# Performance work log

Hardware: AMD Instinct MI355X
Metric: run time of the kernel (lower is better)

The kernel has to match this reference:

```python
import jax, jax.numpy as jnp
import numpy as np

N_NODES = 100000
N_EDGES = 1600000
IN_C = 128
HID_C = 128   # 2 * out_channels
OUT_C = 64


def gcn_conv(x, row, col, w, W, b, num_nodes):
    """PyG GCNConv: linear transform, add self-loops (weight 1),
    symmetric degree normalization, scatter-sum aggregation, bias."""
    h = x @ W  # [N, C_out]
    loop = jnp.arange(num_nodes, dtype=row.dtype)
    r = jnp.concatenate([row, loop])
    c = jnp.concatenate([col, loop])
    ew = jnp.concatenate([w, jnp.ones((num_nodes,), dtype=w.dtype)])
    deg = jax.ops.segment_sum(ew, c, num_segments=num_nodes)
    dinv = jnp.where(deg > 0, jax.lax.rsqrt(deg), 0.0)
    norm = dinv[r] * ew * dinv[c]            # [E+N]
    msg = h[r] * norm[:, None]               # [E+N, C_out] gather
    out = jax.ops.segment_sum(msg, c, num_segments=num_nodes)
    return out + b


def setup_inputs() -> dict:
    key = jax.random.key(0)
    k1, k2, k3, k4, k5, k6, k7, k8 = jax.random.split(key, 8)
    x = jax.random.normal(k1, (N_NODES, IN_C), dtype=jnp.float32)
    edge_index = jax.random.randint(k2, (2, N_EDGES), 0, N_NODES, dtype=jnp.int64)
    edge_weight = jax.random.uniform(k3, (N_EDGES,), dtype=jnp.float32)
    s1 = float(np.sqrt(6.0 / (IN_C + HID_C)))
    s2 = float(np.sqrt(6.0 / (HID_C + OUT_C)))
    W1 = jax.random.uniform(k4, (IN_C, HID_C), minval=-s1, maxval=s1, dtype=jnp.float32)
    b1 = jnp.zeros((HID_C,), dtype=jnp.float32)
    W2 = jax.random.uniform(k5, (HID_C, OUT_C), minval=-s2, maxval=s2, dtype=jnp.float32)
    b2 = jnp.zeros((OUT_C,), dtype=jnp.float32)
    return {"x": x, "edge_index": edge_index, "edge_weight": edge_weight,
            "W1": W1, "b1": b1, "W2": W2, "b2": b2}


def reference(x, edge_index, edge_weight, W1, b1, W2, b2):
    row, col = edge_index[0], edge_index[1]
    n = x.shape[0]
    h = jax.nn.relu(gcn_conv(x, row, col, edge_weight, W1, b1, n))
    h = jax.nn.relu(gcn_conv(h, row, col, edge_weight, W2, b2, n))
    return h
```

## Files before the change

kernel.cpp:

```cpp
#include <hip/hip_runtime.h>

#define TPB 256

typedef unsigned int uint32;
typedef unsigned short ushort_t;
typedef __attribute__((ext_vector_type(8))) short bf16x8;
typedef __attribute__((ext_vector_type(4))) float f32x4;

constexpr int NB = 256;
constexpr int B1 = 256;

__device__ __forceinline__ uint32 pack_bf16x2(float a, float b) {
  uint32 ua = __float_as_uint(a), ub = __float_as_uint(b);
  ua += 0x7FFFu + ((ua >> 16) & 1u);
  ub += 0x7FFFu + ((ub >> 16) & 1u);
  return (ua >> 16) | (ub & 0xFFFF0000u);
}
__device__ __forceinline__ ushort_t bf16_of(float a) {
  uint32 u = __float_as_uint(a);
  u += 0x7FFFu + ((u >> 16) & 1u);
  return (ushort_t)(u >> 16);
}
__device__ __forceinline__ float bf16_lo(uint32 u) { return __uint_as_float(u << 16); }
__device__ __forceinline__ float bf16_hi(uint32 u) { return __uint_as_float(u & 0xFFFF0000u); }
__device__ __forceinline__ int edge_src(uint32 e) { return (int)(e >> 15); }
__device__ __forceinline__ float edge_w(uint32 e) { return __uint_as_float((e & 0x7FFFu) << 16); }
__device__ __forceinline__ float ubf0(uint32 u) { return (float)(u & 0xFFu); }
__device__ __forceinline__ float ubf1(uint32 u) { return (float)((u >> 8) & 0xFFu); }
__device__ __forceinline__ float ubf2(uint32 u) { return (float)((u >> 16) & 0xFFu); }
__device__ __forceinline__ float ubf3(uint32 u) { return (float)((u >> 24) & 0xFFu); }

__global__ __launch_bounds__(256) void rx_hist(const int* __restrict__ col,
                                               int* __restrict__ blockhist, int e, int chunk,
                                               const float* __restrict__ W1, ushort_t* __restrict__ Wt1,
                                               const float* __restrict__ W2, ushort_t* __restrict__ Wt2,
                                               const float* __restrict__ b1, float* __restrict__ b1p) {
  __shared__ int h[NB];
  int tid = threadIdx.x, blk = blockIdx.x;
  h[tid] = 0;
  __syncthreads();
  int s = blk * chunk, t = min(e, s + chunk);
  for (int i = s + tid; i < t; i += 256) atomicAdd(&h[col[i] & 255], 1);
  int gtid = blk * 256 + tid;
  if (gtid < 128 * 128) {
    int k = gtid >> 7, m = gtid & 127;
    Wt1[m * 128 + k] = bf16_of(W1[gtid]);
  } else if (gtid < 128 * 128 + 128 * 64) {
    int j = gtid - 128 * 128;
    int k = j >> 6, m = j & 63;
    int kp = ((k & 15) << 3) | (k >> 4);
    Wt2[m * 128 + kp] = bf16_of(W2[j]);
  } else if (gtid < 128 * 128 + 128 * 64 + 128) {
    int p = gtid - (128 * 128 + 128 * 64);
    b1p[p] = b1[16 * (p & 7) + (p >> 3)];
  }
  __syncthreads();
  blockhist[tid * B1 + blk] = h[tid];
}

__global__ __launch_bounds__(256) void k_scan1(int* __restrict__ a, int* __restrict__ bsum, int n) {
  __shared__ int s[256];
  int tid = threadIdx.x;
  int base = blockIdx.x * 1024 + tid * 4;
  int v0 = 0, v1 = 0, v2 = 0, v3 = 0;
  if (base + 0 < n) v0 = a[base + 0];
  if (base + 1 < n) v1 = a[base + 1];
  if (base + 2 < n) v2 = a[base + 2];
  if (base + 3 < n) v3 = a[base + 3];
  int tsum = v0 + v1 + v2 + v3;
  s[tid] = tsum;
  __syncthreads();
  for (int off = 1; off < 256; off <<= 1) {
    int t = (tid >= off) ? s[tid - off] : 0;
    __syncthreads();
    s[tid] += t;
    __syncthreads();
  }
  if (tid == 255) bsum[blockIdx.x] = s[255];
  int e0 = s[tid] - tsum;
  int e1 = e0 + v0, e2 = e1 + v1, e3 = e2 + v2;
  if (base + 0 < n) a[base + 0] = e0;
  if (base + 1 < n) a[base + 1] = e1;
  if (base + 2 < n) a[base + 2] = e2;
  if (base + 3 < n) a[base + 3] = e3;
}

__global__ __launch_bounds__(256) void k_scan2(int* __restrict__ bsum, int nb) {
  __shared__ int s[256];
  int tid = threadIdx.x;
  int v = (tid < nb) ? bsum[tid] : 0;
  s[tid] = v;
  __syncthreads();
  for (int off = 1; off < 256; off <<= 1) {
    int t = (tid >= off) ? s[tid - off] : 0;
    __syncthreads();
    s[tid] += t;
    __syncthreads();
  }
  if (tid < nb) bsum[tid] = s[tid] - v;
}

__global__ __launch_bounds__(256) void rx_scatter1(const int* __restrict__ row,
                                                   const int* __restrict__ col,
                                                   const float* __restrict__ w,
                                                   const int* __restrict__ scanned,
                                                   const int* __restrict__ bsum,
                                                   int2* __restrict__ rec, int e, int chunk) {
  __shared__ int cur[NB];
  int tid = threadIdx.x, blk = blockIdx.x;
  int idx = tid * B1 + blk;
  cur[tid] = scanned[idx] + bsum[idx >> 10];
  __syncthreads();
  int s = blk * chunk, t = min(e, s + chunk);
  for (int i = s + tid; i < t; i += 256) {
    int c = col[i];
    int p = atomicAdd(&cur[c & 255], 1);
    rec[p] = make_int2(row[i] | ((c >> 8) << 20), __float_as_int(w[i]));
  }
}

__global__ __launch_bounds__(256) void rx_build(const int2* __restrict__ rec,
                                                const int* __restrict__ scanned,
                                                const int* __restrict__ bsum,
                                                int2* __restrict__ nodeRange,
                                                float* __restrict__ dinv,
                                                uint32* __restrict__ edges, int n, int e) {
  constexpr int NH = 512;
  __shared__ int cnt[NH];
  __shared__ int pref[NH];
  __shared__ int cur[NH];
  __shared__ float dw[NH];
  __shared__ int ssum[256];
  int tid = threadIdx.x, lo = blockIdx.x;
  int si = lo * B1;
  int s = scanned[si] + bsum[si >> 10];
  int t;
  if (lo == NB - 1) t = e;
  else {
    int ti = (lo + 1) * B1;
    t = scanned[ti] + bsum[ti >> 10];
  }
  cnt[tid] = 0; cnt[tid + 256] = 0;
  dw[tid] = 0.f; dw[tid + 256] = 0.f;
  __syncthreads();
  for (int i = s + tid; i < t; i += 256) {
    int2 r = rec[i];
    int hi = ((uint32)r.x) >> 20;
    atomicAdd(&cnt[hi], 1);
    atomicAdd(&dw[hi], __int_as_float(r.y));
  }
  __syncthreads();
  int a0 = cnt[2 * tid], a1 = cnt[2 * tid + 1];
  int sum2 = a0 + a1;
  ssum[tid] = sum2;
  __syncthreads();
  for (int off = 1; off < 256; off <<= 1) {
    int v = (tid >= off) ? ssum[tid - off] : 0;
    __syncthreads();
    ssum[tid] += v;
    __syncthreads();
  }
  int excl = ssum[tid] - sum2;
  pref[2 * tid] = excl;
  pref[2 * tid + 1] = excl + a0;
  __syncthreads();
#pragma unroll
  for (int k = 0; k < 2; ++k) {
    int hi = tid + k * 256;
    int node = (hi << 8) | lo;
    cur[hi] = s + pref[hi];
    if (node < n) {
      nodeRange[node] = make_int2(s + pref[hi], cnt[hi]);
      dinv[node] = rsqrtf(1.0f + dw[hi]);
    }
  }
  __syncthreads();
  for (int i = s + tid; i < t; i += 256) {
    int2 r = rec[i];
    int hi = ((uint32)r.x) >> 20;
    int p = atomicAdd(&cur[hi], 1);
    uint32 src = (uint32)(r.x & 0x1FFFF);
    uint32 wb = (uint32)bf16_of(__int_as_float(r.y)) & 0x7FFFu;
    edges[p] = (src << 15) | wb;
  }
}

template <int M, bool XF32, bool SWZ>
__global__ __launch_bounds__(256) void k_gemm_q(
    const void* __restrict__ Xv, const ushort_t* __restrict__ Wt,
    const float* __restrict__ dinv, unsigned char* __restrict__ Hb8,
    float* __restrict__ sc, int n) {
  __shared__ __align__(16) char smem[16384 + M * 256];
  char* Xs = smem;
  char* Ws = smem + 16384;
  const int tid = threadIdx.x;
  const int lane = tid & 63;
  const int w = tid >> 6;
  const int row0 = blockIdx.x * 64;

  {
    const uint4* src = (const uint4*)Wt;
    for (int idx = tid; idx < M * 16; idx += 256) {
      int r = idx >> 4, g = idx & 15;
      uint4 v = src[idx];
      *(uint4*)(Ws + ((r << 8) | ((g << 4) ^ ((r & 7) << 4)))) = v;
    }
  }
  if constexpr (XF32) {
    const float4* src = (const float4*)Xv;
    for (int idx = tid; idx < 64 * 16; idx += 256) {
      int r = idx >> 4, g = idx & 15;
      int grow = row0 + r;
      float4 va = make_float4(0.f, 0.f, 0.f, 0.f), vb = va;
      if (grow < n) {
        va = src[(size_t)grow * 32 + g * 2];
        vb = src[(size_t)grow * 32 + g * 2 + 1];
      }
      uint4 p;
      p.x = pack_bf16x2(va.x, va.y);
      p.y = pack_bf16x2(va.z, va.w);
      p.z = pack_bf16x2(vb.x, vb.y);
      p.w = pack_bf16x2(vb.z, vb.w);
      *(uint4*)(Xs + ((r << 8) | ((g << 4) ^ ((r & 7) << 4)))) = p;
    }
  } else {
    const uint4* src = (const uint4*)Xv;
    for (int idx = tid; idx < 64 * 16; idx += 256) {
      int r = idx >> 4, g = idx & 15;
      int grow = row0 + r;
      uint4 v = make_uint4(0u, 0u, 0u, 0u);
      if (grow < n) v = src[(size_t)grow * 16 + g];
      *(uint4*)(Xs + ((r << 8) | ((g << 4) ^ ((r & 7) << 4)))) = v;
    }
  }
  __syncthreads();

  constexpr int CT = M / 16;
  f32x4 acc[CT];
#pragma unroll
  for (int c = 0; c < CT; ++c) acc[c] = (f32x4){0.f, 0.f, 0.f, 0.f};

  const int arow = (w << 4) | (lane & 15);
  const int kb0 = (lane >> 4) << 4;
#pragma unroll
  for (int ks = 0; ks < 4; ++ks) {
    int kbyte = ks * 64 + kb0;
    bf16x8 a = *(const bf16x8*)(Xs + ((arow << 8) | (kbyte ^ ((arow & 7) << 4))));
#pragma unroll
    for (int c = 0; c < CT; ++c) {
      int brow = c * 16 + (lane & 15);
      bf16x8 b = *(const bf16x8*)(Ws + ((brow << 8) | (kbyte ^ ((brow & 7) << 4))));
      acc[c] = __builtin_amdgcn_mfma_f32_16x16x32_bf16(a, b, acc[c], 0, 0, 0);
    }
  }
  __syncthreads();

  const int gl = lane & 15;
  const int rbase = (w << 4) | ((lane >> 4) << 2);
  float mx[4] = {0.f, 0.f, 0.f, 0.f};
#pragma unroll
  for (int r = 0; r < 4; ++r) {
    int g = row0 + rbase + r;
    float dv = (g < n) ? dinv[g] : 0.f;
#pragma unroll
    for (int c = 0; c < CT; ++c) {
      acc[c][r] *= dv;
      mx[r] = fmaxf(mx[r], fabsf(acc[c][r]));
    }
  }
#pragma unroll
  for (int off = 1; off < 16; off <<= 1) {
#pragma unroll
    for (int r = 0; r < 4; ++r) mx[r] = fmaxf(mx[r], __shfl_xor(mx[r], off));
  }
  float inv[4];
#pragma unroll
  for (int r = 0; r < 4; ++r) {
    inv[r] = (mx[r] > 1e-30f) ? 127.0f / mx[r] : 0.f;
    int g = row0 + rbase + r;
    if (g < n && gl == 0) sc[g] = mx[r] * (1.0f / 127.0f);
  }

  if constexpr (SWZ) {
#pragma unroll
    for (int r = 0; r < 4; ++r) {
      int g = row0 + rbase + r;
      if (g >= n) continue;
      uint32 lo = 0, hi = 0;
#pragma unroll
      for (int c = 0; c < 4; ++c) {
        uint32 q = (uint32)((int)rintf(acc[c][r] * inv[r]) + 128);
        lo |= q << (8 * c);
      }
#pragma unroll
      for (int c = 4; c < 8; ++c) {
        uint32 q = (uint32)((int)rintf(acc[c][r] * inv[r]) + 128);
        hi |= q << (8 * (c - 4));
      }
      ((uint2*)Hb8)[(size_t)g * 16 + gl] = make_uint2(lo, hi);
    }
  } else {
    unsigned char* Cs = (unsigned char*)smem;
#pragma unroll
    for (int r = 0; r < 4; ++r) {
#pragma unroll
      for (int c = 0; c < CT; ++c) {
        int q = (int)rintf(acc[c][r] * inv[r]) + 128;
        Cs[(rbase + r) * 68 + c * 16 + gl] = (unsigned char)q;
      }
    }
    __syncthreads();
    for (int idx = tid; idx < 64 * (M / 4); idx += 256) {
      int r = idx / (M / 4), g = idx % (M / 4);
      int grow = row0 + r;
      if (grow < n)
        ((uint32*)Hb8)[(size_t)grow * (M / 4) + g] = *(const uint32*)(Cs + r * 68 + g * 4);
    }
  }
}

__global__ __launch_bounds__(TPB) void k_agg128(
    const uint2* __restrict__ t8, const float* __restrict__ scs,
    const uint32* __restrict__ edges, const int2* __restrict__ nodeRange,
    const float* __restrict__ dinv, const float* __restrict__ b1p,
    uint4* __restrict__ out, int n) {
  __shared__ uint32 ebuf[TPB / 64][64];
  int node = (blockIdx.x * TPB + threadIdx.x) >> 6;
  if (node >= n) return;
  node = __builtin_amdgcn_readfirstlane(node);
  int lane = threadIdx.x & 63;
  int wv = (threadIdx.x >> 6) & (TPB / 64 - 1);
  int g = lane >> 4, gl = lane & 15;
  int2 nr = nodeRange[node];
  int s0 = nr.x, cnt = nr.y;
  int nLds = min(cnt, 64);
  float di = dinv[node];
  if (lane < nLds) ebuf[wv][lane] = __builtin_nontemporal_load(edges + s0 + lane);

  float a0, a1, a2, a3, a4, a5, a6, a7, beta;
  if (g == 0) {
    uint2 u = t8[(size_t)node * 16 + gl];
    float al = scs[node];
    beta = al;
    a0 = ubf0(u.x) * al; a1 = ubf1(u.x) * al; a2 = ubf2(u.x) * al; a3 = ubf3(u.x) * al;
    a4 = ubf0(u.y) * al; a5 = ubf1(u.y) * al; a6 = ubf2(u.y) * al; a7 = ubf3(u.y) * al;
  } else {
    beta = 0.f;
    a0 = a1 = a2 = a3 = a4 = a5 = a6 = a7 = 0.f;
  }
  int k = g;
  for (; k + 12 < nLds; k += 16) {
    uint32 e0 = ebuf[wv][k], e1 = ebuf[wv][k + 4], e2 = ebuf[wv][k + 8], e3 = ebuf[wv][k + 12];
    int r0 = edge_src(e0), r1 = edge_src(e1), r2 = edge_src(e2), r3 = edge_src(e3);
    uint2 v0 = t8[(size_t)r0 * 16 + gl];
    uint2 v1 = t8[(size_t)r1 * 16 + gl];
    uint2 v2 = t8[(size_t)r2 * 16 + gl];
    uint2 v3 = t8[(size_t)r3 * 16 + gl];
    float al0 = edge_w(e0) * scs[r0], al1 = edge_w(e1) * scs[r1];
    float al2 = edge_w(e2) * scs[r2], al3 = edge_w(e3) * scs[r3];
    beta += (al0 + al1) + (al2 + al3);
    a0 = fmaf(ubf0(v0.x), al0, a0); a1 = fmaf(ubf1(v0.x), al0, a1);
    a2 = fmaf(ubf2(v0.x), al0, a2); a3 = fmaf(ubf3(v0.x), al0, a3);
    a4 = fmaf(ubf0(v0.y), al0, a4); a5 = fmaf(ubf1(v0.y), al0, a5);
    a6 = fmaf(ubf2(v0.y), al0, a6); a7 = fmaf(ubf3(v0.y), al0, a7);
    a0 = fmaf(ubf0(v1.x), al1, a0); a1 = fmaf(ubf1(v1.x), al1, a1);
    a2 = fmaf(ubf2(v1.x), al1, a2); a3 = fmaf(ubf3(v1.x), al1, a3);
    a4 = fmaf(ubf0(v1.y), al1, a4); a5 = fmaf(ubf1(v1.y), al1, a5);
    a6 = fmaf(ubf2(v1.y), al1, a6); a7 = fmaf(ubf3(v1.y), al1, a7);
    a0 = fmaf(ubf0(v2.x), al2, a0); a1 = fmaf(ubf1(v2.x), al2, a1);
    a2 = fmaf(ubf2(v2.x), al2, a2); a3 = fmaf(ubf3(v2.x), al2, a3);
    a4 = fmaf(ubf0(v2.y), al2, a4); a5 = fmaf(ubf1(v2.y), al2, a5);
    a6 = fmaf(ubf2(v2.y), al2, a6); a7 = fmaf(ubf3(v2.y), al2, a7);
    a0 = fmaf(ubf0(v3.x), al3, a0); a1 = fmaf(ubf1(v3.x), al3, a1);
    a2 = fmaf(ubf2(v3.x), al3, a2); a3 = fmaf(ubf3(v3.x), al3, a3);
    a4 = fmaf(ubf0(v3.y), al3, a4); a5 = fmaf(ubf1(v3.y), al3, a5);
    a6 = fmaf(ubf2(v3.y), al3, a6); a7 = fmaf(ubf3(v3.y), al3, a7);
  }
  for (; k < nLds; k += 4) {
    uint32 e0 = ebuf[wv][k];
    int r0 = edge_src(e0);
    uint2 v0 = t8[(size_t)r0 * 16 + gl];
    float al0 = edge_w(e0) * scs[r0];
    beta += al0;
    a0 = fmaf(ubf0(v0.x), al0, a0); a1 = fmaf(ubf1(v0.x), al0, a1);
    a2 = fmaf(ubf2(v0.x), al0, a2); a3 = fmaf(ubf3(v0.x), al0, a3);
    a4 = fmaf(ubf0(v0.y), al0, a4); a5 = fmaf(ubf1(v0.y), al0, a5);
    a6 = fmaf(ubf2(v0.y), al0, a6); a7 = fmaf(ubf3(v0.y), al0, a7);
  }
  for (int kk = s0 + 64 + g; kk < s0 + cnt; kk += 4) {
    uint32 e0 = edges[kk];
    int r0 = edge_src(e0);
    uint2 v0 = t8[(size_t)r0 * 16 + gl];
    float al0 = edge_w(e0) * scs[r0];
    beta += al0;
    a0 = fmaf(ubf0(v0.x), al0, a0); a1 = fmaf(ubf1(v0.x), al0, a1);
    a2 = fmaf(ubf2(v0.x), al0, a2); a3 = fmaf(ubf3(v0.x), al0, a3);
    a4 = fmaf(ubf0(v0.y), al0, a4); a5 = fmaf(ubf1(v0.y), al0, a5);
    a6 = fmaf(ubf2(v0.y), al0, a6); a7 = fmaf(ubf3(v0.y), al0, a7);
  }
  a0 += __shfl_xor(a0, 16); a1 += __shfl_xor(a1, 16);
  a2 += __shfl_xor(a2, 16); a3 += __shfl_xor(a3, 16);
  a4 += __shfl_xor(a4, 16); a5 += __shfl_xor(a5, 16);
  a6 += __shfl_xor(a6, 16); a7 += __shfl_xor(a7, 16);
  beta += __shfl_xor(beta, 16);
  a0 += __shfl_xor(a0, 32); a1 += __shfl_xor(a1, 32);
  a2 += __shfl_xor(a2, 32); a3 += __shfl_xor(a3, 32);
  a4 += __shfl_xor(a4, 32); a5 += __shfl_xor(a5, 32);
  a6 += __shfl_xor(a6, 32); a7 += __shfl_xor(a7, 32);
  beta += __shfl_xor(beta, 32);
  if (g == 0) {
    float corr = 128.0f * beta;
    float4 bb0 = ((const float4*)b1p)[gl * 2];
    float4 bb1 = ((const float4*)b1p)[gl * 2 + 1];
    float o0 = fmaxf(fmaf(a0 - corr, di, bb0.x), 0.f);
    float o1 = fmaxf(fmaf(a1 - corr, di, bb0.y), 0.f);
    float o2 = fmaxf(fmaf(a2 - corr, di, bb0.z), 0.f);
    float o3 = fmaxf(fmaf(a3 - corr, di, bb0.w), 0.f);
    float o4 = fmaxf(fmaf(a4 - corr, di, bb1.x), 0.f);
    float o5 = fmaxf(fmaf(a5 - corr, di, bb1.y), 0.f);
    float o6 = fmaxf(fmaf(a6 - corr, di, bb1.z), 0.f);
    float o7 = fmaxf(fmaf(a7 - corr, di, bb1.w), 0.f);
    uint4 ob;
    ob.x = pack_bf16x2(o0, o1);
    ob.y = pack_bf16x2(o2, o3);
    ob.z = pack_bf16x2(o4, o5);
    ob.w = pack_bf16x2(o6, o7);
    out[(size_t)node * 16 + gl] = ob;
  }
}

__global__ __launch_bounds__(TPB) void k_agg64(
    const uint2* __restrict__ t8, const float* __restrict__ scs,
    const uint32* __restrict__ edges, const int2* __restrict__ nodeRange,
    const float* __restrict__ dinv, const float* __restrict__ bias,
    float4* __restrict__ out, int n) {
  __shared__ uint32 ebuf[TPB / 64][64];
  int node = (blockIdx.x * TPB + threadIdx.x) >> 6;
  if (node >= n) return;
  node = __builtin_amdgcn_readfirstlane(node);
  int lane = threadIdx.x & 63;
  int wv = (threadIdx.x >> 6) & (TPB / 64 - 1);
  int g = lane >> 3, gl = lane & 7;
  int2 nr = nodeRange[node];
  int s0 = nr.x, cnt = nr.y;
  int nLds = min(cnt, 64);
  float di = dinv[node];
  if (lane < nLds) ebuf[wv][lane] = __builtin_nontemporal_load(edges + s0 + lane);

  float a0, a1, a2, a3, a4, a5, a6, a7, beta;
  if (g == 0) {
    uint2 u = t8[(size_t)node * 8 + gl];
    float al = scs[node];
    beta = al;
    a0 = ubf0(u.x) * al; a1 = ubf1(u.x) * al; a2 = ubf2(u.x) * al; a3 = ubf3(u.x) * al;
    a4 = ubf0(u.y) * al; a5 = ubf1(u.y) * al; a6 = ubf2(u.y) * al; a7 = ubf3(u.y) * al;
  } else {
    beta = 0.f;
    a0 = a1 = a2 = a3 = a4 = a5 = a6 = a7 = 0.f;
  }
  int k = g;
  for (; k + 8 < nLds; k += 16) {
    uint32 e0 = ebuf[wv][k], e1 = ebuf[wv][k + 8];
    int r0 = edge_src(e0), r1 = edge_src(e1);
    uint2 v0 = t8[(size_t)r0 * 8 + gl];
    uint2 v1 = t8[(size_t)r1 * 8 + gl];
    float al0 = edge_w(e0) * scs[r0], al1 = edge_w(e1) * scs[r1];
    beta += al0 + al1;
    a0 = fmaf(ubf0(v0.x), al0, a0); a1 = fmaf(ubf1(v0.x), al0, a1);
    a2 = fmaf(ubf2(v0.x), al0, a2); a3 = fmaf(ubf3(v0.x), al0, a3);
    a4 = fmaf(ubf0(v0.y), al0, a4); a5 = fmaf(ubf1(v0.y), al0, a5);
    a6 = fmaf(ubf2(v0.y), al0, a6); a7 = fmaf(ubf3(v0.y), al0, a7);
    a0 = fmaf(ubf0(v1.x), al1, a0); a1 = fmaf(ubf1(v1.x), al1, a1);
    a2 = fmaf(ubf2(v1.x), al1, a2); a3 = fmaf(ubf3(v1.x), al1, a3);
    a4 = fmaf(ubf0(v1.y), al1, a4); a5 = fmaf(ubf1(v1.y), al1, a5);
    a6 = fmaf(ubf2(v1.y), al1, a6); a7 = fmaf(ubf3(v1.y), al1, a7);
  }
  for (; k < nLds; k += 8) {
    uint32 e0 = ebuf[wv][k];
    int r0 = edge_src(e0);
    uint2 v0 = t8[(size_t)r0 * 8 + gl];
    float al0 = edge_w(e0) * scs[r0];
    beta += al0;
    a0 = fmaf(ubf0(v0.x), al0, a0); a1 = fmaf(ubf1(v0.x), al0, a1);
    a2 = fmaf(ubf2(v0.x), al0, a2); a3 = fmaf(ubf3(v0.x), al0, a3);
    a4 = fmaf(ubf0(v0.y), al0, a4); a5 = fmaf(ubf1(v0.y), al0, a5);
    a6 = fmaf(ubf2(v0.y), al0, a6); a7 = fmaf(ubf3(v0.y), al0, a7);
  }
  for (int kk = s0 + 64 + g; kk < s0 + cnt; kk += 8) {
    uint32 e0 = edges[kk];
    int r0 = edge_src(e0);
    uint2 v0 = t8[(size_t)r0 * 8 + gl];
    float al0 = edge_w(e0) * scs[r0];
    beta += al0;
    a0 = fmaf(ubf0(v0.x), al0, a0); a1 = fmaf(ubf1(v0.x), al0, a1);
    a2 = fmaf(ubf2(v0.x), al0, a2); a3 = fmaf(ubf3(v0.x), al0, a3);
    a4 = fmaf(ubf0(v0.y), al0, a4); a5 = fmaf(ubf1(v0.y), al0, a5);
    a6 = fmaf(ubf2(v0.y), al0, a6); a7 = fmaf(ubf3(v0.y), al0, a7);
  }
#pragma unroll
  for (int off = 8; off <= 32; off <<= 1) {
    a0 += __shfl_xor(a0, off); a1 += __shfl_xor(a1, off);
    a2 += __shfl_xor(a2, off); a3 += __shfl_xor(a3, off);
    a4 += __shfl_xor(a4, off); a5 += __shfl_xor(a5, off);
    a6 += __shfl_xor(a6, off); a7 += __shfl_xor(a7, off);
    beta += __shfl_xor(beta, off);
  }
  if (g == 0) {
    float corr = 128.0f * beta;
    float4 bb0 = ((const float4*)bias)[gl * 2];
    float4 bb1 = ((const float4*)bias)[gl * 2 + 1];
    float4 o0, o1;
    o0.x = fmaxf(fmaf(a0 - corr, di, bb0.x), 0.f);
    o0.y = fmaxf(fmaf(a1 - corr, di, bb0.y), 0.f);
    o0.z = fmaxf(fmaf(a2 - corr, di, bb0.z), 0.f);
    o0.w = fmaxf(fmaf(a3 - corr, di, bb0.w), 0.f);
    o1.x = fmaxf(fmaf(a4 - corr, di, bb1.x), 0.f);
    o1.y = fmaxf(fmaf(a5 - corr, di, bb1.y), 0.f);
    o1.z = fmaxf(fmaf(a6 - corr, di, bb1.z), 0.f);
    o1.w = fmaxf(fmaf(a7 - corr, di, bb1.w), 0.f);
    out[(size_t)node * 16 + gl * 2] = o0;
    out[(size_t)node * 16 + gl * 2 + 1] = o1;
  }
}

extern "C" void kernel_launch(void* const* d_in, const int* in_sizes, int n_in,
                              void* d_out, int out_size, void* d_ws, size_t ws_size,
                              hipStream_t stream) {
  const float* x  = (const float*)d_in[0];
  const int*   ei = (const int*)d_in[1];
  const float* ew = (const float*)d_in[2];
  const float* W1 = (const float*)d_in[3];
  const float* b1 = (const float*)d_in[4];
  const float* W2 = (const float*)d_in[5];
  const float* b2 = (const float*)d_in[6];
  float* out = (float*)d_out;

  constexpr int IN_C = 128, HID = 128, OUTC = 64;
  const int n = in_sizes[0] / IN_C;
  const int e = in_sizes[2];
  const int* rowp = ei;
  const int* colp = ei + e;

  auto cdiv = [](long a, long b) { return (int)((a + b - 1) / b); };
  auto align = [](size_t v) { return (v + 255) & ~(size_t)255; };

  char* ws = (char*)d_ws;
  size_t o = 0;
  int*      blockhist = (int*)(ws + o);      o = align(o + (size_t)NB * B1 * 4);
  int*      bsum      = (int*)(ws + o);      o = align(o + 4096);
  float*    dinv      = (float*)(ws + o);    o = align(o + (size_t)n * 4);
  int2*     nodeRange = (int2*)(ws + o);     o = align(o + (size_t)n * 8);
  ushort_t* Wt1       = (ushort_t*)(ws + o); o = align(o + (size_t)HID * IN_C * 2);
  ushort_t* Wt2       = (ushort_t*)(ws + o); o = align(o + (size_t)OUTC * HID * 2);
  float*    b1p       = (float*)(ws + o);    o = align(o + 512);
  float*    sc1       = (float*)(ws + o);    o = align(o + (size_t)n * 4);
  float*    sc2       = (float*)(ws + o);    o = align(o + (size_t)n * 4);
  int2*     rec       = (int2*)(ws + o);     o = align(o + (size_t)e * 8);
  uint32*   edges     = (uint32*)(ws + o);   o = align(o + (size_t)e * 4);
  unsigned char* hs1b8 = (unsigned char*)(ws + o); o = align(o + (size_t)n * HID);
  uint4*    o1b       = (uint4*)(ws + o);    o = align(o + (size_t)n * HID * 2);
  unsigned char* hs2b8 = hs1b8;

  const int chunk = cdiv(e, B1);
  const int nscan = NB * B1;

  rx_hist<<<B1, 256, 0, stream>>>(colp, blockhist, e, chunk, W1, Wt1, W2, Wt2, b1, b1p);
  k_scan1<<<nscan / 1024, 256, 0, stream>>>(blockhist, bsum, nscan);
  k_scan2<<<1, 256, 0, stream>>>(bsum, nscan / 1024);
  rx_scatter1<<<B1, 256, 0, stream>>>(rowp, colp, ew, blockhist, bsum, rec, e, chunk);
  rx_build<<<NB, 256, 0, stream>>>(rec, blockhist, bsum, nodeRange, dinv, edges, n, e);

  k_gemm_q<HID, true, true><<<cdiv(n, 64), 256, 0, stream>>>(x, Wt1, dinv, hs1b8, sc1, n);
  k_agg128<<<cdiv(n, 4), TPB, 0, stream>>>((const uint2*)hs1b8, sc1, edges, nodeRange,
                                           dinv, b1p, o1b, n);

  k_gemm_q<OUTC, false, false><<<cdiv(n, 64), 256, 0, stream>>>(o1b, Wt2, dinv, hs2b8, sc2, n);
  k_agg64<<<cdiv(n, 4), TPB, 0, stream>>>((const uint2*)hs2b8, sc2, edges, nodeRange,
                                          dinv, b2, (float4*)out, n);
}
```

Before: 193.9 us.

## Merge two-pass scan into one kernel and replace LDS edge buffer with shuffles

Replaces the two-kernel block-sum scan of the radix histogram with a single 1024-thread kernel. Each thread serially scans a 64-element segment, which removes one launch and the bsum indirection in the scatter and build kernels. In both aggregation kernels, the per-wave LDS edge buffer is replaced by a register-held edge word broadcast with __shfl, and the tail loop is folded into a padded main loop. Padded slots use edge 0, so this relies on edge 0 decoding to zero weight. The single-block scan also serialises 64 dependent global loads per thread.

```diff
diff --git a/kernel.cpp b/kernel.cpp
--- a/kernel.cpp
+++ b/kernel.cpp
@@ -58,58 +58,37 @@
   blockhist[tid * B1 + blk] = h[tid];
 }
 
-__global__ __launch_bounds__(256) void k_scan1(int* __restrict__ a, int* __restrict__ bsum, int n) {
-  __shared__ int s[256];
+__global__ __launch_bounds__(1024) void k_scan_one(int* __restrict__ a, int n) {
+  __shared__ int s[1024];
   int tid = threadIdx.x;
-  int base = blockIdx.x * 1024 + tid * 4;
-  int v0 = 0, v1 = 0, v2 = 0, v3 = 0;
-  if (base + 0 < n) v0 = a[base + 0];
-  if (base + 1 < n) v1 = a[base + 1];
-  if (base + 2 < n) v2 = a[base + 2];
-  if (base + 3 < n) v3 = a[base + 3];
-  int tsum = v0 + v1 + v2 + v3;
-  s[tid] = tsum;
-  __syncthreads();
-  for (int off = 1; off < 256; off <<= 1) {
+  int per = n >> 10;
+  int base = tid * per;
+  int sum = 0;
+  for (int i = 0; i < per; ++i) sum += a[base + i];
+  s[tid] = sum;
+  __syncthreads();
+  for (int off = 1; off < 1024; off <<= 1) {
     int t = (tid >= off) ? s[tid - off] : 0;
     __syncthreads();
     s[tid] += t;
     __syncthreads();
   }
-  if (tid == 255) bsum[blockIdx.x] = s[255];
-  int e0 = s[tid] - tsum;
-  int e1 = e0 + v0, e2 = e1 + v1, e3 = e2 + v2;
-  if (base + 0 < n) a[base + 0] = e0;
-  if (base + 1 < n) a[base + 1] = e1;
-  if (base + 2 < n) a[base + 2] = e2;
-  if (base + 3 < n) a[base + 3] = e3;
-}
-
-__global__ __launch_bounds__(256) void k_scan2(int* __restrict__ bsum, int nb) {
-  __shared__ int s[256];
-  int tid = threadIdx.x;
-  int v = (tid < nb) ? bsum[tid] : 0;
-  s[tid] = v;
-  __syncthreads();
-  for (int off = 1; off < 256; off <<= 1) {
-    int t = (tid >= off) ? s[tid - off] : 0;
-    __syncthreads();
-    s[tid] += t;
-    __syncthreads();
-  }
-  if (tid < nb) bsum[tid] = s[tid] - v;
+  int run = s[tid] - sum;
+  for (int i = 0; i < per; ++i) {
+    int t = a[base + i];
+    a[base + i] = run;
+    run += t;
+  }
 }
 
 __global__ __launch_bounds__(256) void rx_scatter1(const int* __restrict__ row,
                                                    const int* __restrict__ col,
                                                    const float* __restrict__ w,
                                                    const int* __restrict__ scanned,
-                                                   const int* __restrict__ bsum,
                                                    int2* __restrict__ rec, int e, int chunk) {
   __shared__ int cur[NB];
   int tid = threadIdx.x, blk = blockIdx.x;
-  int idx = tid * B1 + blk;
-  cur[tid] = scanned[idx] + bsum[idx >> 10];
+  cur[tid] = scanned[tid * B1 + blk];
   __syncthreads();
   int s = blk * chunk, t = min(e, s + chunk);
   for (int i = s + tid; i < t; i += 256) {
@@ -121,7 +100,6 @@
 
 __global__ __launch_bounds__(256) void rx_build(const int2* __restrict__ rec,
                                                 const int* __restrict__ scanned,
-                                                const int* __restrict__ bsum,
                                                 int2* __restrict__ nodeRange,
                                                 float* __restrict__ dinv,
                                                 uint32* __restrict__ edges, int n, int e) {
@@ -132,14 +110,8 @@
   __shared__ float dw[NH];
   __shared__ int ssum[256];
   int tid = threadIdx.x, lo = blockIdx.x;
-  int si = lo * B1;
-  int s = scanned[si] + bsum[si >> 10];
-  int t;
-  if (lo == NB - 1) t = e;
-  else {
-    int ti = (lo + 1) * B1;
-    t = scanned[ti] + bsum[ti >> 10];
-  }
+  int s = scanned[lo * B1];
+  int t = (lo == NB - 1) ? e : scanned[(lo + 1) * B1];
   cnt[tid] = 0; cnt[tid + 256] = 0;
   dw[tid] = 0.f; dw[tid + 256] = 0.f;
   __syncthreads();
@@ -324,18 +296,16 @@
     const uint32* __restrict__ edges, const int2* __restrict__ nodeRange,
     const float* __restrict__ dinv, const float* __restrict__ b1p,
     uint4* __restrict__ out, int n) {
-  __shared__ uint32 ebuf[TPB / 64][64];
   int node = (blockIdx.x * TPB + threadIdx.x) >> 6;
   if (node >= n) return;
   node = __builtin_amdgcn_readfirstlane(node);
   int lane = threadIdx.x & 63;
-  int wv = (threadIdx.x >> 6) & (TPB / 64 - 1);
   int g = lane >> 4, gl = lane & 15;
   int2 nr = nodeRange[node];
   int s0 = nr.x, cnt = nr.y;
-  int nLds = min(cnt, 64);
+  int nS = min(cnt, 64);
   float di = dinv[node];
-  if (lane < nLds) ebuf[wv][lane] = __builtin_nontemporal_load(edges + s0 + lane);
+  uint32 ev = (lane < nS) ? edges[s0 + lane] : 0u;
 
   float a0, a1, a2, a3, a4, a5, a6, a7, beta;
   if (g == 0) {
@@ -348,9 +318,11 @@
     beta = 0.f;
     a0 = a1 = a2 = a3 = a4 = a5 = a6 = a7 = 0.f;
   }
+  int iters = (nS + 15) >> 4;
   int k = g;
-  for (; k + 12 < nLds; k += 16) {
-    uint32 e0 = ebuf[wv][k], e1 = ebuf[wv][k + 4], e2 = ebuf[wv][k + 8], e3 = ebuf[wv][k + 12];
+  for (int it = 0; it < iters; ++it, k += 16) {
+    uint32 e0 = __shfl(ev, k), e1 = __shfl(ev, k + 4);
+    uint32 e2 = __shfl(ev, k + 8), e3 = __shfl(ev, k + 12);
     int r0 = edge_src(e0), r1 = edge_src(e1), r2 = edge_src(e2), r3 = edge_src(e3);
     uint2 v0 = t8[(size_t)r0 * 16 + gl];
     uint2 v1 = t8[(size_t)r1 * 16 + gl];
@@ -375,17 +347,6 @@
     a2 = fmaf(ubf2(v3.x), al3, a2); a3 = fmaf(ubf3(v3.x), al3, a3);
     a4 = fmaf(ubf0(v3.y), al3, a4); a5 = fmaf(ubf1(v3.y), al3, a5);
     a6 = fmaf(ubf2(v3.y), al3, a6); a7 = fmaf(ubf3(v3.y), al3, a7);
-  }
-  for (; k < nLds; k += 4) {
-    uint32 e0 = ebuf[wv][k];
-    int r0 = edge_src(e0);
-    uint2 v0 = t8[(size_t)r0 * 16 + gl];
-    float al0 = edge_w(e0) * scs[r0];
-    beta += al0;
-    a0 = fmaf(ubf0(v0.x), al0, a0); a1 = fmaf(ubf1(v0.x), al0, a1);
-    a2 = fmaf(ubf2(v0.x), al0, a2); a3 = fmaf(ubf3(v0.x), al0, a3);
-    a4 = fmaf(ubf0(v0.y), al0, a4); a5 = fmaf(ubf1(v0.y), al0, a5);
-    a6 = fmaf(ubf2(v0.y), al0, a6); a7 = fmaf(ubf3(v0.y), al0, a7);
   }
   for (int kk = s0 + 64 + g; kk < s0 + cnt; kk += 4) {
     uint32 e0 = edges[kk];
@@ -434,18 +395,16 @@
     const uint32* __restrict__ edges, const int2* __restrict__ nodeRange,
     const float* __restrict__ dinv, const float* __restrict__ bias,
     float4* __restrict__ out, int n) {
-  __shared__ uint32 ebuf[TPB / 64][64];
   int node = (blockIdx.x * TPB + threadIdx.x) >> 6;
   if (node >= n) return;
   node = __builtin_amdgcn_readfirstlane(node);
   int lane = threadIdx.x & 63;
-  int wv = (threadIdx.x >> 6) & (TPB / 64 - 1);
   int g = lane >> 3, gl = lane & 7;
   int2 nr = nodeRange[node];
   int s0 = nr.x, cnt = nr.y;
-  int nLds = min(cnt, 64);
+  int nS = min(cnt, 64);
   float di = dinv[node];
-  if (lane < nLds) ebuf[wv][lane] = __builtin_nontemporal_load(edges + s0 + lane);
+  uint32 ev = (lane < nS) ? edges[s0 + lane] : 0u;
 
   float a0, a1, a2, a3, a4, a5, a6, a7, beta;
   if (g == 0) {
@@ -458,9 +417,10 @@
     beta = 0.f;
     a0 = a1 = a2 = a3 = a4 = a5 = a6 = a7 = 0.f;
   }
+  int iters = (nS + 15) >> 4;
   int k = g;
-  for (; k + 8 < nLds; k += 16) {
-    uint32 e0 = ebuf[wv][k], e1 = ebuf[wv][k + 8];
+  for (int it = 0; it < iters; ++it, k += 16) {
+    uint32 e0 = __shfl(ev, k), e1 = __shfl(ev, k + 8);
     int r0 = edge_src(e0), r1 = edge_src(e1);
     uint2 v0 = t8[(size_t)r0 * 8 + gl];
     uint2 v1 = t8[(size_t)r1 * 8 + gl];
@@ -474,17 +434,6 @@
     a2 = fmaf(ubf2(v1.x), al1, a2); a3 = fmaf(ubf3(v1.x), al1, a3);
     a4 = fmaf(ubf0(v1.y), al1, a4); a5 = fmaf(ubf1(v1.y), al1, a5);
     a6 = fmaf(ubf2(v1.y), al1, a6); a7 = fmaf(ubf3(v1.y), al1, a7);
-  }
-  for (; k < nLds; k += 8) {
-    uint32 e0 = ebuf[wv][k];
-    int r0 = edge_src(e0);
-    uint2 v0 = t8[(size_t)r0 * 8 + gl];
-    float al0 = edge_w(e0) * scs[r0];
-    beta += al0;
-    a0 = fmaf(ubf0(v0.x), al0, a0); a1 = fmaf(ubf1(v0.x), al0, a1);
-    a2 = fmaf(ubf2(v0.x), al0, a2); a3 = fmaf(ubf3(v0.x), al0, a3);
-    a4 = fmaf(ubf0(v0.y), al0, a4); a5 = fmaf(ubf1(v0.y), al0, a5);
-    a6 = fmaf(ubf2(v0.y), al0, a6); a7 = fmaf(ubf3(v0.y), al0, a7);
   }
   for (int kk = s0 + 64 + g; kk < s0 + cnt; kk += 8) {
     uint32 e0 = edges[kk];
@@ -547,7 +496,6 @@
   char* ws = (char*)d_ws;
   size_t o = 0;
   int*      blockhist = (int*)(ws + o);      o = align(o + (size_t)NB * B1 * 4);
-  int*      bsum      = (int*)(ws + o);      o = align(o + 4096);
   float*    dinv      = (float*)(ws + o);    o = align(o + (size_t)n * 4);
   int2*     nodeRange = (int2*)(ws + o);     o = align(o + (size_t)n * 8);
   ushort_t* Wt1       = (ushort_t*)(ws + o); o = align(o + (size_t)HID * IN_C * 2);
@@ -565,10 +513,9 @@
   const int nscan = NB * B1;
 
   rx_hist<<<B1, 256, 0, stream>>>(colp, blockhist, e, chunk, W1, Wt1, W2, Wt2, b1, b1p);
-  k_scan1<<<nscan / 1024, 256, 0, stream>>>(blockhist, bsum, nscan);
-  k_scan2<<<1, 256, 0, stream>>>(bsum, nscan / 1024);
-  rx_scatter1<<<B1, 256, 0, stream>>>(rowp, colp, ew, blockhist, bsum, rec, e, chunk);
-  rx_build<<<NB, 256, 0, stream>>>(rec, blockhist, bsum, nodeRange, dinv, edges, n, e);
+  k_scan_one<<<1, 1024, 0, stream>>>(blockhist, nscan);
+  rx_scatter1<<<B1, 256, 0, stream>>>(rowp, colp, ew, blockhist, rec, e, chunk);
+  rx_build<<<NB, 256, 0, stream>>>(rec, blockhist, nodeRange, dinv, edges, n, e);
 
   k_gemm_q<HID, true, true><<<cdiv(n, 64), 256, 0, stream>>>(x, Wt1, dinv, hs1b8, sc1, n);
   k_agg128<<<cdiv(n, 4), TPB, 0, stream>>>((const uint2*)hs1b8, sc1, edges, nodeRange,
```

Result: slower. 267.6 us (+38.0%).
